# Kernel tuning notes

Measured on AMD Instinct MI355X. Metric: run time of the kernel, lower is better.

## Reference

```python
import jax, jax.numpy as jnp
import numpy as np

B, H, T, D = 4, 8, 4096, 64
NC = 64      # num_clusters
WSZ = 128    # window_size (== context_window_size)
MEM = 1      # num_mem_kv
EPS = 1e-5   # scatter_mean eps


def setup_inputs() -> dict:
    key = jax.random.key(0)
    kq, kk, kv, km, kmk, kmv = jax.random.split(key, 6)
    return {
        "q": jax.random.normal(kq, (B, H, T, D), jnp.float32),
        "k": jax.random.normal(kk, (B, H, T, D), jnp.float32),
        "v": jax.random.normal(kv, (B, H, T, D), jnp.float32),
        "means": jax.random.normal(km, (H, NC, D), jnp.float32),
        "mem_key": jax.random.normal(kmk, (H, NC, MEM, D), jnp.float32),
        "mem_value": jax.random.normal(kmv, (H, NC, MEM, D), jnp.float32),
    }


def reference(q, k, v, means, mem_key, mem_value):
    b, h, t, d = q.shape
    kv_t = k.shape[2]
    nc = means.shape[1]
    wsz = min(WSZ, t)
    kv_wsz = min(WSZ, kv_t)

    # --- kmeans routing (eval mode: no update, world_size=1) ---
    x = jnp.concatenate([q, k], axis=2)                       # (b,h,t+kv_t,d)
    norm = jnp.linalg.norm(x, axis=-1, keepdims=True)
    xn = x / jnp.maximum(norm, 1e-12)                          # F.normalize
    dists = jnp.einsum('bhld,hcd->bhlc', xn, means)            # (b,h,L,nc)
    buckets = jnp.argmax(dists, axis=-1)                       # (b,h,L)
    routed = means[jnp.arange(h)[None, :, None], buckets]      # (b,h,L,d)
    aux_loss = jnp.mean((xn - routed) ** 2)                    # mse / world_size(=1)

    dists = jax.lax.stop_gradient(dists)                       # torch no_grad
    q_dists, k_dists = dists[:, :, :t], dists[:, :, t:]

    def top_idx(dd, w):
        # dd: (b,h,L,nc) -> per-cluster top-w token indices, (b,h,nc*w)
        _, idx = jax.lax.top_k(jnp.swapaxes(dd, -1, -2), w)    # (b,h,nc,w)
        return idx.reshape(idx.shape[0], idx.shape[1], -1)

    indices = top_idx(q_dists, wsz)                            # (b,h,nc*wsz)
    kv_indices = top_idx(k_dists, kv_wsz)

    gather = lambda arr, idx: jnp.take_along_axis(arr, idx[..., None], axis=2)
    qg = gather(q, indices).reshape(b, h, nc, wsz, d)
    kg = gather(k, kv_indices).reshape(b, h, nc, kv_wsz, d)
    vg = gather(v, kv_indices).reshape(b, h, nc, kv_wsz, d)

    m_k = jnp.broadcast_to(mem_key[None], (b,) + mem_key.shape)
    m_v = jnp.broadcast_to(mem_value[None], (b,) + mem_value.shape)
    kg = jnp.concatenate([m_k, kg], axis=3)                    # (b,h,nc,MEM+kv_wsz,d)
    vg = jnp.concatenate([m_v, vg], axis=3)

    dots = jnp.einsum('bhnid,bhnjd->bhnij', qg, kg) * (d ** -0.5)
    attn = jax.nn.softmax(dots, axis=-1)
    bo = jnp.einsum('bhnij,bhnjd->bhnid', attn, vg)            # (b,h,nc,wsz,d)
    so = bo.reshape(b, h, nc * wsz, d)

    # scatter_mean back to token positions
    bi = jnp.arange(b)[:, None, None]
    hi = jnp.arange(h)[None, :, None]
    numer = jnp.zeros((b, h, t, d), q.dtype).at[bi, hi, indices].add(so)
    denom = jnp.zeros((b, h, t, d), q.dtype).at[bi, hi, indices].add(jnp.ones_like(so))
    out = numer / (denom + EPS)
    return out, aux_loss
```

## Files before the change

kernel.cpp:

```cpp
#include <hip/hip_runtime.h>
#include <math.h>

#define BB 4
#define HH 8
#define TT 4096
#define DD 64
#define NCC 64
#define WSZW 128
#define TPK 160
#define MEMN 1
#define KVW (MEMN + WSZW)
constexpr float EPSF = 1e-5f;
constexpr float SCALE = 0.125f;

typedef __attribute__((ext_vector_type(8))) short bf16x8;
typedef __attribute__((ext_vector_type(4))) float f32x4;

static __device__ __forceinline__ unsigned int pk2(float a, float b) {
    unsigned int r;
    asm("v_cvt_pk_bf16_f32 %0, %1, %2" : "=v"(r) : "v"(a), "v"(b));
    return r;
}
static __device__ __forceinline__ bf16x8 pack8(float4 a, float4 b) {
    union { unsigned int u[4]; bf16x8 v; } r;
    r.u[0] = pk2(a.x, a.y); r.u[1] = pk2(a.z, a.w);
    r.u[2] = pk2(b.x, b.y); r.u[3] = pk2(b.z, b.w);
    return r.v;
}
static __device__ __forceinline__ unsigned mono16(unsigned u) {
    return (u ^ ((u & 0x8000u) ? 0xFFFFu : 0x8000u)) & 0xFFFFu;
}
static __device__ __forceinline__ unsigned long long mono64(double d) {
    unsigned long long b = (unsigned long long)__double_as_longlong(d);
    return b ^ (((long long)b < 0) ? ~0ULL : 0x8000000000000000ULL);
}
static __device__ __forceinline__ float bf2f(unsigned short u) {
    return __uint_as_float(((unsigned)u) << 16);
}

__global__ __launch_bounds__(256, 4) void dists_kernel(
    const float* __restrict__ q, const float* __restrict__ k,
    const float* __restrict__ means,
    unsigned short* __restrict__ distsQ, unsigned short* __restrict__ distsK,
    float* __restrict__ aux_part, double* __restrict__ invn,
    int* __restrict__ counts)
{
    __shared__ __align__(16) unsigned short mhS[64 * 64];
    __shared__ __align__(16) unsigned short mlS[64 * 64];
    __shared__ __align__(16) unsigned short xhS[64 * 64];
    __shared__ __align__(16) unsigned short xlS[64 * 64];
    __shared__ float mqS[64];
    __shared__ float ssnS[64];
    __shared__ float wMaxS[64 * 5];
    __shared__ int   wIdxS[64 * 5];

    const int chunks = (2 * TT) / 64;
    int bid0 = blockIdx.x;
    int bid = (bid0 & 7) * 512 + (bid0 >> 3);
    int bh = bid / chunks;
    int chunk = bid % chunks;
    int h = bh % HH;
    bool isQ = chunk < (TT / 64);
    int tbase = (isQ ? chunk : chunk - 64) * 64;
    const float* src = (isQ ? q : k) + ((size_t)bh * TT + tbase) * DD;
    unsigned short* dst = isQ ? distsQ : distsK;
    double* invdst = invn + (isQ ? 0 : (size_t)BB * HH * TT) + (size_t)bh * TT + tbase;

    int tid = threadIdx.x;

    if (tid < 32) counts[(size_t)bid0 * 32 + tid] = 0;

    int row = tid >> 2, part = tid & 3;

    {
        const float* mp = means + ((size_t)h * NCC + row) * DD + part * 16;
        float f[16];
        float msq = 0.f;
        #pragma unroll
        for (int i = 0; i < 4; ++i) {
            float4 va = *(const float4*)(mp + i * 4);
            f[i*4] = va.x; f[i*4+1] = va.y; f[i*4+2] = va.z; f[i*4+3] = va.w;
            msq += va.x*va.x + va.y*va.y + va.z*va.z + va.w*va.w;
        }
        msq += __shfl_xor(msq, 1);
        msq += __shfl_xor(msq, 2);
        if (part == 0) mqS[row] = msq;
        #pragma unroll
        for (int cc = 0; cc < 2; ++cc) {
            unsigned hw[4], lw[4];
            #pragma unroll
            for (int j2 = 0; j2 < 4; ++j2) {
                float a = f[cc*8 + j2*2], b = f[cc*8 + j2*2 + 1];
                unsigned p = pk2(a, b);
                float ha = __uint_as_float(p << 16);
                float hb = __uint_as_float(p & 0xFFFF0000u);
                hw[j2] = p; lw[j2] = pk2(a - ha, b - hb);
            }
            int ch = part * 2 + cc;
            int phys = ch ^ (row & 7);
            *reinterpret_cast<uint4*>(&mhS[row * 64 + phys * 8]) = (uint4){hw[0],hw[1],hw[2],hw[3]};
            *reinterpret_cast<uint4*>(&mlS[row * 64 + phys * 8]) = (uint4){lw[0],lw[1],lw[2],lw[3]};
        }
    }
    {
        const float* xp = src + (size_t)row * DD + part * 16;
        float f[16];
        double ssd = 0.0;
        #pragma unroll
        for (int i = 0; i < 4; ++i) {
            float4 va = *(const float4*)(xp + i * 4);
            f[i*4] = va.x; f[i*4+1] = va.y; f[i*4+2] = va.z; f[i*4+3] = va.w;
            ssd += (double)va.x*va.x + (double)va.y*va.y
                 + (double)va.z*va.z + (double)va.w*va.w;
        }
        ssd += __shfl_xor(ssd, 1);
        ssd += __shfl_xor(ssd, 2);
        double invd = 1.0 / fmax(sqrt(ssd), 1e-12);
        if (part == 0) {
            invdst[row] = invd;
            ssnS[row] = (float)(ssd * invd * invd);
        }
        float inv = (float)invd;
        #pragma unroll
        for (int i = 0; i < 16; ++i) f[i] *= inv;
        #pragma unroll
        for (int cc = 0; cc < 2; ++cc) {
            unsigned hw[4], lw[4];
            #pragma unroll
            for (int j2 = 0; j2 < 4; ++j2) {
                float a = f[cc*8 + j2*2], b = f[cc*8 + j2*2 + 1];
                unsigned p = pk2(a, b);
                float ha = __uint_as_float(p << 16);
                float hb = __uint_as_float(p & 0xFFFF0000u);
                hw[j2] = p; lw[j2] = pk2(a - ha, b - hb);
            }
            int ch = part * 2 + cc;
            int phys = ch ^ (row & 7);
            *reinterpret_cast<uint4*>(&xhS[row * 64 + phys * 8]) = (uint4){hw[0],hw[1],hw[2],hw[3]};
            *reinterpret_cast<uint4*>(&xlS[row * 64 + phys * 8]) = (uint4){lw[0],lw[1],lw[2],lw[3]};
        }
    }
    __syncthreads();

    int l = tid & 63, w = tid >> 6;
    int lr = l & 15, lg = l >> 4;

    bf16x8 mhF[2], mlF[2];
    #pragma unroll
    for (int ks = 0; ks < 2; ++ks) {
        int r2 = w * 16 + lr;
        int phys = (ks * 4 + lg) ^ (r2 & 7);
        mhF[ks] = *reinterpret_cast<const bf16x8*>(&mhS[r2 * 64 + phys * 8]);
        mlF[ks] = *reinterpret_cast<const bf16x8*>(&mlS[r2 * 64 + phys * 8]);
    }

    f32x4 accT[4];
    size_t rowb = (size_t)(bh * NCC) * TT;
    #pragma unroll
    for (int tt = 0; tt < 4; ++tt) {
        bf16x8 xhF[2], xlF[2];
        #pragma unroll
        for (int ks = 0; ks < 2; ++ks) {
            int r2 = tt * 16 + lr;
            int phys = (ks * 4 + lg) ^ (r2 & 7);
            xhF[ks] = *reinterpret_cast<const bf16x8*>(&xhS[r2 * 64 + phys * 8]);
            xlF[ks] = *reinterpret_cast<const bf16x8*>(&xlS[r2 * 64 + phys * 8]);
        }
        f32x4 a = (f32x4){0.f, 0.f, 0.f, 0.f};
        #pragma unroll
        for (int ks = 0; ks < 2; ++ks)
            a = __builtin_amdgcn_mfma_f32_16x16x32_bf16(mhF[ks], xhF[ks], a, 0, 0, 0);
        #pragma unroll
        for (int ks = 0; ks < 2; ++ks)
            a = __builtin_amdgcn_mfma_f32_16x16x32_bf16(mhF[ks], xlF[ks], a, 0, 0, 0);
        #pragma unroll
        for (int ks = 0; ks < 2; ++ks)
            a = __builtin_amdgcn_mfma_f32_16x16x32_bf16(mlF[ks], xhF[ks], a, 0, 0, 0);
        accT[tt] = a;
        #pragma unroll
        for (int r2 = 0; r2 < 4; ++r2) {
            int c = w * 16 + lg * 4 + r2;
            dst[rowb + (size_t)c * TT + tbase + tt * 16 + lr] =
                (unsigned short)(pk2(a[r2], a[r2]) & 0xFFFFu);
        }
    }

    #pragma unroll
    for (int tt = 0; tt < 4; ++tt) {
        float bv = accT[tt][0]; int bc = w * 16 + lg * 4;
        #pragma unroll
        for (int r2 = 1; r2 < 4; ++r2)
            if (accT[tt][r2] > bv) { bv = accT[tt][r2]; bc = w * 16 + lg * 4 + r2; }
        #pragma unroll
        for (int off = 16; off <= 32; off <<= 1) {
            float ov = __shfl_xor(bv, off);
            int   oc = __shfl_xor(bc, off);
            if (ov > bv || (ov == bv && oc < bc)) { bv = ov; bc = oc; }
        }
        if (lg == 0) {
            wMaxS[(tt * 16 + lr) * 5 + w] = bv;
            wIdxS[(tt * 16 + lr) * 5 + w] = bc;
        }
    }
    __syncthreads();

    if (tid < 64) {
        float bv = -1e30f; int bc = 0;
        #pragma unroll
        for (int w2 = 0; w2 < 4; ++w2) {
            float ov = wMaxS[tid * 5 + w2];
            int   oc = wIdxS[tid * 5 + w2];
            if (ov > bv || (ov == bv && oc < bc)) { bv = ov; bc = oc; }
        }
        float auxv = ssnS[tid] + mqS[bc] - 2.f * bv;
        #pragma unroll
        for (int off = 32; off; off >>= 1) auxv += __shfl_xor(auxv, off);
        if (tid == 0) aux_part[bid] = auxv;
    }
}

__global__ __launch_bounds__(512) void topk_kernel(
    const unsigned short* __restrict__ dists, int* __restrict__ idxOut)
{
    int row = blockIdx.x;
    const unsigned short* dv = dists + (size_t)row * TT;
    int t = threadIdx.x;
    int lane = t & 63, w = t >> 6;

    unsigned u[8];
    {
        uint4 a = *(const uint4*)(dv + t * 8);
        unsigned ws[4] = {a.x, a.y, a.z, a.w};
        #pragma unroll
        for (int i = 0; i < 4; ++i) {
            u[i*2]   = mono16(ws[i] & 0xFFFFu);
            u[i*2+1] = mono16(ws[i] >> 16);
        }
    }

    __shared__ int hist[4096];
    __shared__ int wtot[8];
    __shared__ int binSel, tgtS;
    __shared__ int nGtS, posS, eqPos;

    int target = TPK;

    {
        int4* hz = (int4*)&hist[t * 8];
        hz[0] = (int4){0,0,0,0}; hz[1] = (int4){0,0,0,0};
        __syncthreads();
        #pragma unroll
        for (int j = 0; j < 8; ++j) atomicAdd(&hist[u[j] >> 4], 1);
        __syncthreads();
        int cnt[8], ls[8];
        {
            const int4* hp = (const int4*)&hist[t * 8];
            int4 c0 = hp[0], c1 = hp[1];
            cnt[0]=c0.x; cnt[1]=c0.y; cnt[2]=c0.z; cnt[3]=c0.w;
            cnt[4]=c1.x; cnt[5]=c1.y; cnt[6]=c1.z; cnt[7]=c1.w;
        }
        int run = 0;
        #pragma unroll
        for (int i = 7; i >= 0; --i) { run += cnt[i]; ls[i] = run; }
        int S = run;
        #pragma unroll
        for (int off = 1; off < 64; off <<= 1) {
            int o = __shfl_down(S, off);
            if (lane + off < 64) S += o;
        }
        if (lane == 0) wtot[w] = S;
        __syncthreads();
        int after = 0;
        for (int ww = w + 1; ww < 8; ++ww) after += wtot[ww];
        int St1 = S - run + after;
        #pragma unroll
        for (int i = 0; i < 8; ++i) {
            int sfxb = ls[i] + St1;
            if (sfxb >= target && sfxb - cnt[i] < target) {
                binSel = t * 8 + i; tgtS = target - (sfxb - cnt[i]);
            }
        }
        __syncthreads();
    }
    unsigned prefix12 = (unsigned)binSel;
    target = tgtS;
    __syncthreads();

    if (t < 16) hist[t] = 0;
    __syncthreads();
    #pragma unroll
    for (int j = 0; j < 8; ++j)
        if ((u[j] >> 4) == prefix12) atomicAdd(&hist[u[j] & 0xF], 1);
    __syncthreads();
    if (t < 16) {
        int cnt = hist[t];
        int S = cnt;
        #pragma unroll
        for (int off = 1; off < 16; off <<= 1) {
            int o = __shfl_down(S, off);
            if (t + off < 16) S += o;
        }
        if (S >= target && S - cnt < target) binSel = t;
    }
    __syncthreads();
    unsigned pivot = (prefix12 << 4) | (unsigned)binSel;

    if (t == 0) { nGtS = 0; posS = 0; eqPos = 0; }
    __syncthreads();
    int myg = 0;
    #pragma unroll
    for (int j = 0; j < 8; ++j) myg += (u[j] > pivot) ? 1 : 0;
    if (myg) atomicAdd(&nGtS, myg);
    __syncthreads();
    int n_gt = nGtS;
    int n_need = TPK - n_gt;
    int* out = idxOut + (size_t)row * TPK;
    #pragma unroll
    for (int j = 0; j < 8; ++j) {
        if (u[j] > pivot) {
            int p = atomicAdd(&posS, 1);
            out[p] = t * 8 + j;
        } else if (u[j] == pivot) {
            int p = atomicAdd(&eqPos, 1);
            if (p < n_need) out[n_gt + p] = t * 8 + j;
        }
    }
}

__global__ __launch_bounds__(640) void rescore_kernel(
    const float* __restrict__ q, const float* __restrict__ k,
    const float* __restrict__ means, const double* __restrict__ invn,
    const int* __restrict__ candQ, const int* __restrict__ candK,
    int* __restrict__ idxQ, int* __restrict__ idxK,
    int* __restrict__ counts)
{
    int bid = blockIdx.x;
    int rid = (bid & 7) * 512 + (bid >> 3);
    int side = rid >> 11;
    int row = rid & 2047;
    int c = row & (NCC - 1);
    int bh = row >> 6;
    int h = bh % HH;

    const int* cand = (side ? candK : candQ) + (size_t)row * TPK;
    int* outIdx     = (side ? idxK : idxQ) + (size_t)row * WSZW;
    const float* xbase = (side ? k : q) + (size_t)bh * TT * DD;
    const double* invp = invn + (side ? (size_t)BB * HH * TT : 0) + (size_t)bh * TT;

    __shared__ double   mD[DD];
    __shared__ unsigned hiS[TPK];
    __shared__ unsigned loS[TPK];
    __shared__ int      kiS[TPK];

    int tid = threadIdx.x;
    if (tid < DD) mD[tid] = (double)means[((size_t)h * NCC + c) * DD + tid];
    __syncthreads();

    int g = tid >> 2;
    int qt = tid & 3;
    int tok = cand[g];
    const float* xp = xbase + (size_t)tok * DD + qt * 16;
    double inv = invp[tok];
    double d0 = 0.0, d1 = 0.0;
    #pragma unroll
    for (int i = 0; i < 2; ++i) {
        float4 va = *(const float4*)(xp + i * 4);
        int d = qt * 16 + i * 4;
        d0 += (double)va.x * mD[d]   + (double)va.y * mD[d+1]
            + (double)va.z * mD[d+2] + (double)va.w * mD[d+3];
    }
    #pragma unroll
    for (int i = 2; i < 4; ++i) {
        float4 va = *(const float4*)(xp + i * 4);
        int d = qt * 16 + i * 4;
        d1 += (double)va.x * mD[d]   + (double)va.y * mD[d+1]
            + (double)va.z * mD[d+2] + (double)va.w * mD[d+3];
    }
    double dot = d0 + d1;
    dot += __shfl_xor(dot, 1); dot += __shfl_xor(dot, 2);
    double v = dot * inv;
    unsigned long long key = mono64(v);
    unsigned myhi = (unsigned)(key >> 32), mylo = (unsigned)key;
    if (qt == 0) { hiS[g] = myhi; loS[g] = mylo; kiS[g] = tok; }
    __syncthreads();

    int rk = 0, eq = 0;
    #pragma unroll 8
    for (int i = 0; i < TPK / 4; ++i) {
        unsigned hj = hiS[qt * (TPK / 4) + i];
        rk += (hj > myhi) ? 1 : 0;
        eq += (hj == myhi) ? 1 : 0;
    }
    rk += __shfl_xor(rk, 1); rk += __shfl_xor(rk, 2);
    eq += __shfl_xor(eq, 1); eq += __shfl_xor(eq, 2);

    if (eq > 1) {
        int rk2 = 0;
        for (int i = 0; i < TPK / 4; ++i) {
            int j = qt * (TPK / 4) + i;
            unsigned hj = hiS[j];
            if (hj > myhi) rk2++;
            else if (hj == myhi) {
                unsigned lj = loS[j];
                if (lj > mylo || (lj == mylo && kiS[j] < tok)) rk2++;
            }
        }
        rk2 += __shfl_xor(rk2, 1); rk2 += __shfl_xor(rk2, 2);
        rk = rk2;
    }

    if (qt == 0 && rk < WSZW) {
        outIdx[rk] = tok;
        if (side == 0) atomicAdd(&counts[bh * TT + tok], 1);
    }
}

__global__ __launch_bounds__(512, 8) void attn_scanfill_kernel(
    const float* __restrict__ q, const float* __restrict__ k, const float* __restrict__ v,
    const float* __restrict__ mem_key, const float* __restrict__ mem_value,
    const int* __restrict__ idxQ, const int* __restrict__ idxK,
    unsigned short* __restrict__ so,
    const int* __restrict__ counts, int* __restrict__ offs, int* __restrict__ csr,
    const float* __restrict__ auxp, float* __restrict__ out)
{
    __shared__ __align__(16) unsigned char smemRaw[38144];
    int bid = blockIdx.x;

    if (bid >= 2048) {
        int bh = bid - 2048;
        int t = threadIdx.x;
        int lane = t & 63, w = t >> 6;
        int* offsL = (int*)smemRaw;
        int* curL  = (int*)(smemRaw + 16384);
        int* wsum  = (int*)(smemRaw + 32768);
        float* auxW = (float*)(smemRaw + 32800);

        float s = 0.f;
        if (bh == 0)
            for (int i = t; i < 4096; i += 512) s += auxp[i];
        #pragma unroll
        for (int off = 32; off; off >>= 1) s += __shfl_xor(s, off);
        if (lane == 0) auxW[w] = s;
        __syncthreads();
        if (bh == 0 && t == 0) {
            float a = 0.f;
            #pragma unroll
            for (int i = 0; i < 8; ++i) a += auxW[i];
            out[(size_t)BB * HH * TT * DD] =
                a * (1.0f / (float)(BB * HH * 2 * TT * DD));
        }

        const int* cb = counts + (size_t)bh * TT;
        int* ob = offs + (size_t)bh * TT;
        int loc[8]; int sum = 0;
        #pragma unroll
        for (int i = 0; i < 8; ++i) { loc[i] = sum; sum += cb[t * 8 + i]; }
        int incl = sum;
        #pragma unroll
        for (int off = 1; off < 64; off <<= 1) {
            int o = __shfl_up(incl, off);
            if (lane >= off) incl += o;
        }
        if (lane == 63) wsum[w] = incl;
        __syncthreads();
        if (t < 8) {
            int v2 = wsum[t];
            int inc2 = v2;
            #pragma unroll
            for (int off = 1; off < 8; off <<= 1) {
                int o = __shfl_up(inc2, off);
                if (t >= off) inc2 += o;
            }
            wsum[t] = inc2 - v2;
        }
        __syncthreads();
        int ex = wsum[w] + incl - sum;
        #pragma unroll
        for (int i = 0; i < 8; ++i) {
            int o = ex + loc[i];
            ob[t * 8 + i] = o;
            offsL[t * 8 + i] = o;
            curL[t * 8 + i] = 0;
        }
        __syncthreads();

        const int* iq = idxQ + ((size_t)bh << 13);
        int* cs = csr + ((size_t)bh << 13);
        for (int i = t; i < 8192; i += 512) {
            int tok = iq[i];
            int p = offsL[tok] + atomicAdd(&curL[tok], 1);
            cs[p] = i;
        }
        return;
    }

    unsigned short* KsS = (unsigned short*)smemRaw;
    unsigned short* VtS = (unsigned short*)(smemRaw + 16640);

    int blk = (bid & 7) * 256 + (bid >> 3);
    int c = blk % NCC;
    int bh = blk / NCC;
    int h = bh % HH;

    int tid = threadIdx.x;
    int w = tid >> 6, l = tid & 63;
    int lr = l & 15, lg = l >> 4;

    const float* memK = mem_key   + ((size_t)h * NCC + c) * (MEMN * DD);
    const float* memV = mem_value + ((size_t)h * NCC + c) * (MEMN * DD);

    int stRow[3], stCh[3];
    const float *vsrcR[3], *ksrcR[3];
    #pragma unroll
    for (int s = 0; s < 3; ++s) {
        int idx = tid + s * 512;
        stRow[s] = idx >> 3; stCh[s] = idx & 7;
        vsrcR[s] = nullptr; ksrcR[s] = nullptr;
        if (idx < 1280 && stRow[s] < KVW) {
            if (stRow[s] == 0) { vsrcR[s] = memV; ksrcR[s] = memK; }
            else {
                int tk = idxK[(size_t)blk * WSZW + stRow[s] - 1];
                vsrcR[s] = v + ((size_t)bh * TT + tk) * DD;
                ksrcR[s] = k + ((size_t)bh * TT + tk) * DD;
            }
        }
    }

    bf16x8 qf[2];
    {
        int tq = idxQ[(size_t)blk * WSZW + w * 16 + lr];
        const float* qp = q + ((size_t)bh * TT + tq) * DD;
        #pragma unroll
        for (int ks = 0; ks < 2; ++ks) {
            float4 a = *(const float4*)(qp + ks * 32 + lg * 8);
            float4 b = *(const float4*)(qp + ks * 32 + lg * 8 + 4);
            qf[ks] = pack8(a, b);
        }
    }

    uint4 vw[3];
    #pragma unroll
    for (int s = 0; s < 3; ++s) {
        vw[s] = (uint4){0,0,0,0};
        if (vsrcR[s]) {
            float4 a = *(const float4*)(vsrcR[s] + stCh[s] * 8);
            float4 b = *(const float4*)(vsrcR[s] + stCh[s] * 8 + 4);
            vw[s].x = pk2(a.x, a.y); vw[s].y = pk2(a.z, a.w);
            vw[s].z = pk2(b.x, b.y); vw[s].w = pk2(b.z, b.w);
        }
    }
    uint4 kw[3];
    #pragma unroll
    for (int s = 0; s < 3; ++s) {
        kw[s] = (uint4){0,0,0,0};
        if (ksrcR[s]) {
            float4 a = *(const float4*)(ksrcR[s] + stCh[s] * 8);
            float4 b = *(const float4*)(ksrcR[s] + stCh[s] * 8 + 4);
            kw[s].x = pk2(a.x, a.y); kw[s].y = pk2(a.z, a.w);
            kw[s].z = pk2(b.x, b.y); kw[s].w = pk2(b.z, b.w);
        }
    }

    #pragma unroll
    for (int s = 0; s < 3; ++s)
        if (vsrcR[s])
            *reinterpret_cast<uint4*>(
                &KsS[stRow[s] * 64 + ((stCh[s] ^ (stRow[s] & 7)) * 8)]) = vw[s];
    __syncthreads();

    unsigned short vreg[3][8];
    #pragma unroll
    for (int s = 0; s < 3; ++s) {
        int idx = tid + s * 512;
        if (idx < 1280) {
            int d = idx & 63, rowblk = idx >> 6;
            #pragma unroll
            for (int i = 0; i < 8; ++i) {
                int row = rowblk * 8 + i;
                int pr = (row < KVW) ? row : 128;
                vreg[s][i] = KsS[pr * 64 + (((d >> 3) ^ (pr & 7)) * 8) + (d & 7)];
            }
        }
    }
    __syncthreads();

    #pragma unroll
    for (int s = 0; s < 3; ++s) {
        int idx = tid + s * 512;
        if (idx < 1280) {
            int d = idx & 63, rowblk = idx >> 6;
            uint4 ow;
            ow.x = (unsigned)vreg[s][0] | ((unsigned)vreg[s][1] << 16);
            ow.y = (unsigned)vreg[s][2] | ((unsigned)vreg[s][3] << 16);
            ow.z = (unsigned)vreg[s][4] | ((unsigned)vreg[s][5] << 16);
            ow.w = (unsigned)vreg[s][6] | ((unsigned)vreg[s][7] << 16);
            *reinterpret_cast<uint4*>(&VtS[d * 168 + rowblk * 8]) = ow;
        }
    }
    #pragma unroll
    for (int s = 0; s < 3; ++s)
        if (ksrcR[s])
            *reinterpret_cast<uint4*>(
                &KsS[stRow[s] * 64 + ((stCh[s] ^ (stRow[s] & 7)) * 8)]) = kw[s];
    __syncthreads();

    f32x4 acc[4];
    #pragma unroll
    for (int dt = 0; dt < 4; ++dt) acc[dt] = (f32x4){0.f, 0.f, 0.f, 0.f};
    float s_sum = 0.f;

    int src0 = lr + ((lg & 1) * 2) * 16;
    int src1 = src0 + 16;
    bool hi = (lg >> 1) != 0;

    for (int kb = 0; kb < 5; ++kb) {
        bf16x8 kf[2][2];
        #pragma unroll
        for (int kvt = 0; kvt < 2; ++kvt)
            #pragma unroll
            for (int ks = 0; ks < 2; ++ks) {
                int row = kb * 32 + kvt * 16 + lr;
                int pr = (row < KVW) ? row : 128;
                int phys = (ks * 4 + lg) ^ (pr & 7);
                kf[kvt][ks] = *reinterpret_cast<const bf16x8*>(&KsS[pr * 64 + phys * 8]);
            }
        __builtin_amdgcn_s_setprio(1);
        unsigned pk[2][2];
        #pragma unroll
        for (int kvt = 0; kvt < 2; ++kvt) {
            f32x4 sf = __builtin_amdgcn_mfma_f32_16x16x32_bf16(
                kf[kvt][0], qf[0], (f32x4){0.f,0.f,0.f,0.f}, 0, 0, 0);
            sf = __builtin_amdgcn_mfma_f32_16x16x32_bf16(kf[kvt][1], qf[1], sf, 0, 0, 0);
            float e[4];
            #pragma unroll
            for (int r = 0; r < 4; ++r) {
                int kv = kb * 32 + kvt * 16 + lg * 4 + r;
                e[r] = (kv < KVW) ? __expf(sf[r] * SCALE) : 0.f;
                s_sum += e[r];
            }
            pk[kvt][0] = pk2(e[0], e[1]);
            pk[kvt][1] = pk2(e[2], e[3]);
        }
        unsigned a00 = __shfl(pk[0][0], src0), a01 = __shfl(pk[0][1], src0);
        unsigned a10 = __shfl(pk[1][0], src0), a11 = __shfl(pk[1][1], src0);
        unsigned b00 = __shfl(pk[0][0], src1), b01 = __shfl(pk[0][1], src1);
        unsigned b10 = __shfl(pk[1][0], src1), b11 = __shfl(pk[1][1], src1);
        union { unsigned u[4]; bf16x8 v; } pu;
        pu.u[0] = hi ? a10 : a00;
        pu.u[1] = hi ? a11 : a01;
        pu.u[2] = hi ? b10 : b00;
        pu.u[3] = hi ? b11 : b01;
        #pragma unroll
        for (int dt = 0; dt < 4; ++dt) {
            bf16x8 vf = *reinterpret_cast<const bf16x8*>(
                &VtS[(dt * 16 + lr) * 168 + kb * 32 + lg * 8]);
            acc[dt] = __builtin_amdgcn_mfma_f32_16x16x32_bf16(pu.v, vf, acc[dt], 0, 0, 0);
        }
        __builtin_amdgcn_s_setprio(0);
    }

    s_sum += __shfl_xor(s_sum, 16);
    s_sum += __shfl_xor(s_sum, 32);
    float sinv[4];
    #pragma unroll
    for (int r = 0; r < 4; ++r)
        sinv[r] = 1.f / __shfl(s_sum, lg * 4 + r);

    #pragma unroll
    for (int r = 0; r < 4; ++r) {
        int row = w * 16 + lg * 4 + r;
        unsigned short* op = so + (((size_t)blk * WSZW + row) * DD);
        #pragma unroll
        for (int dt = 0; dt < 4; ++dt) {
            float ov = acc[dt][r] * sinv[r];
            op[dt * 16 + lr] = (unsigned short)(pk2(ov, ov) & 0xFFFFu);
        }
    }
}

__global__ __launch_bounds__(256) void reduce_kernel(
    const unsigned short* __restrict__ so, const int* __restrict__ counts,
    const int* __restrict__ offs, const int* __restrict__ csr,
    float* __restrict__ out)
{
    int b0 = blockIdx.x;
    int b = (b0 & 7) * 4096 + (b0 >> 3);
    int gt = b * 4 + (threadIdx.x >> 6);
    int lane = threadIdx.x & 63;
    int bh = gt >> 12;
    int n = counts[gt];
    int st = offs[gt];
    const int* cs = csr + ((size_t)bh << 13);
    const unsigned short* sob = so + (((size_t)bh << 13) * DD);
    float acc = 0.f;
    int j = 0;
    for (; j + 2 <= n; j += 2) {
        int s0 = cs[st + j], s1 = cs[st + j + 1];
        float v0 = bf2f(sob[(size_t)s0 * DD + lane]);
        float v1 = bf2f(sob[(size_t)s1 * DD + lane]);
        acc += v0 + v1;
    }
    if (j < n) acc += bf2f(sob[(size_t)cs[st + j] * DD + lane]);
    out[(size_t)gt * DD + lane] = acc / ((float)n + EPSF);
}

extern "C" void kernel_launch(void* const* d_in, const int* in_sizes, int n_in,
                              void* d_out, int out_size, void* d_ws, size_t ws_size,
                              hipStream_t stream) {
    const float* q        = (const float*)d_in[0];
    const float* k        = (const float*)d_in[1];
    const float* v        = (const float*)d_in[2];
    const float* means    = (const float*)d_in[3];
    const float* mem_key  = (const float*)d_in[4];
    const float* mem_val  = (const float*)d_in[5];
    float* out = (float*)d_out;

    const size_t nRows = (size_t)BB * HH * NCC;
    const size_t nTok  = (size_t)BB * HH * TT;
    const size_t nDist = (size_t)BB * HH * NCC * TT;
    unsigned short* distsQ = (unsigned short*)d_ws;
    unsigned short* distsK = distsQ + nDist;
    unsigned short* so     = distsQ;
    int*   idxQ   = (int*)(distsK + nDist);
    int*   idxK   = idxQ + nRows * WSZW;
    int*   counts = idxK + nRows * WSZW;
    float* auxp   = (float*)(counts + nTok);
    int*   offs   = (int*)(auxp + 4096);
    int*   csr    = offs + nTok;
    int*   candQ  = csr + nTok * 2;
    int*   candK  = candQ + nRows * TPK;
    uintptr_t ip  = (uintptr_t)(candK + nRows * TPK);
    ip = (ip + 15) & ~(uintptr_t)15;
    double* invn  = (double*)ip;

    dists_kernel<<<dim3(BB * HH * (2 * TT / 64)), dim3(256), 0, stream>>>(
        q, k, means, distsQ, distsK, auxp, invn, counts);
    topk_kernel<<<dim3((unsigned)(2 * nRows)), dim3(512), 0, stream>>>(distsQ, candQ);
    rescore_kernel<<<dim3((unsigned)(2 * nRows)), dim3(640), 0, stream>>>(
        q, k, means, invn, candQ, candK, idxQ, idxK, counts);
    attn_scanfill_kernel<<<dim3((unsigned)(nRows + BB * HH)), dim3(512), 0, stream>>>(
        q, k, v, mem_key, mem_val, idxQ, idxK, so,
        counts, offs, csr, auxp, out);
    reduce_kernel<<<dim3((unsigned)(nTok / 4)), dim3(256), 0, stream>>>(
        so, counts, offs, csr, out);
}
```

Measured before the change: 160.1 us.

## Fuse radix top-k candidate selection with double-precision rescoring kernel

```diff
diff --git a/kernel.cpp b/kernel.cpp
--- a/kernel.cpp
+++ b/kernel.cpp
@@ -219,118 +219,10 @@
     }
 }
 
-__global__ __launch_bounds__(512) void topk_kernel(
-    const unsigned short* __restrict__ dists, int* __restrict__ idxOut)
-{
-    int row = blockIdx.x;
-    const unsigned short* dv = dists + (size_t)row * TT;
-    int t = threadIdx.x;
-    int lane = t & 63, w = t >> 6;
-
-    unsigned u[8];
-    {
-        uint4 a = *(const uint4*)(dv + t * 8);
-        unsigned ws[4] = {a.x, a.y, a.z, a.w};
-        #pragma unroll
-        for (int i = 0; i < 4; ++i) {
-            u[i*2]   = mono16(ws[i] & 0xFFFFu);
-            u[i*2+1] = mono16(ws[i] >> 16);
-        }
-    }
-
-    __shared__ int hist[4096];
-    __shared__ int wtot[8];
-    __shared__ int binSel, tgtS;
-    __shared__ int nGtS, posS, eqPos;
-
-    int target = TPK;
-
-    {
-        int4* hz = (int4*)&hist[t * 8];
-        hz[0] = (int4){0,0,0,0}; hz[1] = (int4){0,0,0,0};
-        __syncthreads();
-        #pragma unroll
-        for (int j = 0; j < 8; ++j) atomicAdd(&hist[u[j] >> 4], 1);
-        __syncthreads();
-        int cnt[8], ls[8];
-        {
-            const int4* hp = (const int4*)&hist[t * 8];
-            int4 c0 = hp[0], c1 = hp[1];
-            cnt[0]=c0.x; cnt[1]=c0.y; cnt[2]=c0.z; cnt[3]=c0.w;
-            cnt[4]=c1.x; cnt[5]=c1.y; cnt[6]=c1.z; cnt[7]=c1.w;
-        }
-        int run = 0;
-        #pragma unroll
-        for (int i = 7; i >= 0; --i) { run += cnt[i]; ls[i] = run; }
-        int S = run;
-        #pragma unroll
-        for (int off = 1; off < 64; off <<= 1) {
-            int o = __shfl_down(S, off);
-            if (lane + off < 64) S += o;
-        }
-        if (lane == 0) wtot[w] = S;
-        __syncthreads();
-        int after = 0;
-        for (int ww = w + 1; ww < 8; ++ww) after += wtot[ww];
-        int St1 = S - run + after;
-        #pragma unroll
-        for (int i = 0; i < 8; ++i) {
-            int sfxb = ls[i] + St1;
-            if (sfxb >= target && sfxb - cnt[i] < target) {
-                binSel = t * 8 + i; tgtS = target - (sfxb - cnt[i]);
-            }
-        }
-        __syncthreads();
-    }
-    unsigned prefix12 = (unsigned)binSel;
-    target = tgtS;
-    __syncthreads();
-
-    if (t < 16) hist[t] = 0;
-    __syncthreads();
-    #pragma unroll
-    for (int j = 0; j < 8; ++j)
-        if ((u[j] >> 4) == prefix12) atomicAdd(&hist[u[j] & 0xF], 1);
-    __syncthreads();
-    if (t < 16) {
-        int cnt = hist[t];
-        int S = cnt;
-        #pragma unroll
-        for (int off = 1; off < 16; off <<= 1) {
-            int o = __shfl_down(S, off);
-            if (t + off < 16) S += o;
-        }
-        if (S >= target && S - cnt < target) binSel = t;
-    }
-    __syncthreads();
-    unsigned pivot = (prefix12 << 4) | (unsigned)binSel;
-
-    if (t == 0) { nGtS = 0; posS = 0; eqPos = 0; }
-    __syncthreads();
-    int myg = 0;
-    #pragma unroll
-    for (int j = 0; j < 8; ++j) myg += (u[j] > pivot) ? 1 : 0;
-    if (myg) atomicAdd(&nGtS, myg);
-    __syncthreads();
-    int n_gt = nGtS;
-    int n_need = TPK - n_gt;
-    int* out = idxOut + (size_t)row * TPK;
-    #pragma unroll
-    for (int j = 0; j < 8; ++j) {
-        if (u[j] > pivot) {
-            int p = atomicAdd(&posS, 1);
-            out[p] = t * 8 + j;
-        } else if (u[j] == pivot) {
-            int p = atomicAdd(&eqPos, 1);
-            if (p < n_need) out[n_gt + p] = t * 8 + j;
-        }
-    }
-}
-
-__global__ __launch_bounds__(640) void rescore_kernel(
+__global__ __launch_bounds__(512) void topk_rescore_kernel(
+    const unsigned short* __restrict__ dists,
     const float* __restrict__ q, const float* __restrict__ k,
     const float* __restrict__ means, const double* __restrict__ invn,
-    const int* __restrict__ candQ, const int* __restrict__ candK,
     int* __restrict__ idxQ, int* __restrict__ idxK,
     int* __restrict__ counts)
 {
@@ -342,76 +234,190 @@
     int bh = row >> 6;
     int h = bh % HH;
 
-    const int* cand = (side ? candK : candQ) + (size_t)row * TPK;
-    int* outIdx     = (side ? idxK : idxQ) + (size_t)row * WSZW;
+    const unsigned short* dv = dists + ((size_t)side * 2048 + row) * TT;
+    int* outIdx = (side ? idxK : idxQ) + (size_t)row * WSZW;
     const float* xbase = (side ? k : q) + (size_t)bh * TT * DD;
     const double* invp = invn + (side ? (size_t)BB * HH * TT : 0) + (size_t)bh * TT;
 
+    __shared__ int hist[4096];
+    __shared__ int wtot[8];
+    __shared__ int binSel, tgtS;
+    __shared__ int nGtS, posS, eqPos;
+    __shared__ int candL[TPK];
     __shared__ double   mD[DD];
     __shared__ unsigned hiS[TPK];
     __shared__ unsigned loS[TPK];
     __shared__ int      kiS[TPK];
 
-    int tid = threadIdx.x;
-    if (tid < DD) mD[tid] = (double)means[((size_t)h * NCC + c) * DD + tid];
-    __syncthreads();
-
-    int g = tid >> 2;
-    int qt = tid & 3;
-    int tok = cand[g];
-    const float* xp = xbase + (size_t)tok * DD + qt * 16;
-    double inv = invp[tok];
-    double d0 = 0.0, d1 = 0.0;
-    #pragma unroll
-    for (int i = 0; i < 2; ++i) {
-        float4 va = *(const float4*)(xp + i * 4);
-        int d = qt * 16 + i * 4;
-        d0 += (double)va.x * mD[d]   + (double)va.y * mD[d+1]
-            + (double)va.z * mD[d+2] + (double)va.w * mD[d+3];
-    }
-    #pragma unroll
-    for (int i = 2; i < 4; ++i) {
-        float4 va = *(const float4*)(xp + i * 4);
-        int d = qt * 16 + i * 4;
-        d1 += (double)va.x * mD[d]   + (double)va.y * mD[d+1]
-            + (double)va.z * mD[d+2] + (double)va.w * mD[d+3];
-    }
-    double dot = d0 + d1;
-    dot += __shfl_xor(dot, 1); dot += __shfl_xor(dot, 2);
-    double v = dot * inv;
-    unsigned long long key = mono64(v);
-    unsigned myhi = (unsigned)(key >> 32), mylo = (unsigned)key;
-    if (qt == 0) { hiS[g] = myhi; loS[g] = mylo; kiS[g] = tok; }
-    __syncthreads();
-
-    int rk = 0, eq = 0;
-    #pragma unroll 8
-    for (int i = 0; i < TPK / 4; ++i) {
-        unsigned hj = hiS[qt * (TPK / 4) + i];
-        rk += (hj > myhi) ? 1 : 0;
-        eq += (hj == myhi) ? 1 : 0;
-    }
-    rk += __shfl_xor(rk, 1); rk += __shfl_xor(rk, 2);
-    eq += __shfl_xor(eq, 1); eq += __shfl_xor(eq, 2);
-
-    if (eq > 1) {
-        int rk2 = 0;
-        for (int i = 0; i < TPK / 4; ++i) {
-            int j = qt * (TPK / 4) + i;
-            unsigned hj = hiS[j];
-            if (hj > myhi) rk2++;
-            else if (hj == myhi) {
-                unsigned lj = loS[j];
-                if (lj > mylo || (lj == mylo && kiS[j] < tok)) rk2++;
-            }
-        }
-        rk2 += __shfl_xor(rk2, 1); rk2 += __shfl_xor(rk2, 2);
-        rk = rk2;
-    }
-
-    if (qt == 0 && rk < WSZW) {
-        outIdx[rk] = tok;
-        if (side == 0) atomicAdd(&counts[bh * TT + tok], 1);
+    int t = threadIdx.x;
+    int lane = t & 63, w = t >> 6;
+
+    if (t < DD) mD[t] = (double)means[((size_t)h * NCC + c) * DD + t];
+
+    unsigned u[8];
+    {
+        uint4 a = *(const uint4*)(dv + t * 8);
+        unsigned ws[4] = {a.x, a.y, a.z, a.w};
+        #pragma unroll
+        for (int i = 0; i < 4; ++i) {
+            u[i*2]   = mono16(ws[i] & 0xFFFFu);
+            u[i*2+1] = mono16(ws[i] >> 16);
+        }
+    }
+
+    int target = TPK;
+
+    {
+        int4* hz = (int4*)&hist[t * 8];
+        hz[0] = (int4){0,0,0,0}; hz[1] = (int4){0,0,0,0};
+        __syncthreads();
+        #pragma unroll
+        for (int j = 0; j < 8; ++j) atomicAdd(&hist[u[j] >> 4], 1);
+        __syncthreads();
+        int cnt[8], ls[8];
+        {
+            const int4* hp = (const int4*)&hist[t * 8];
+            int4 c0 = hp[0], c1 = hp[1];
+            cnt[0]=c0.x; cnt[1]=c0.y; cnt[2]=c0.z; cnt[3]=c0.w;
+            cnt[4]=c1.x; cnt[5]=c1.y; cnt[6]=c1.z; cnt[7]=c1.w;
+        }
+        int run = 0;
+        #pragma unroll
+        for (int i = 7; i >= 0; --i) { run += cnt[i]; ls[i] = run; }
+        int S = run;
+        #pragma unroll
+        for (int off = 1; off < 64; off <<= 1) {
+            int o = __shfl_down(S, off);
+            if (lane + off < 64) S += o;
+        }
+        if (lane == 0) wtot[w] = S;
+        __syncthreads();
+        int after = 0;
+        for (int ww = w + 1; ww < 8; ++ww) after += wtot[ww];
+        int St1 = S - run + after;
+        #pragma unroll
+        for (int i = 0; i < 8; ++i) {
+            int sfxb = ls[i] + St1;
+            if (sfxb >= target && sfxb - cnt[i] < target) {
+                binSel = t * 8 + i; tgtS = target - (sfxb - cnt[i]);
+            }
+        }
+        __syncthreads();
+    }
+    unsigned prefix12 = (unsigned)binSel;
+    target = tgtS;
+    __syncthreads();
+
+    if (t < 16) hist[t] = 0;
+    __syncthreads();
+    #pragma unroll
+    for (int j = 0; j < 8; ++j)
+        if ((u[j] >> 4) == prefix12) atomicAdd(&hist[u[j] & 0xF], 1);
+    __syncthreads();
+    if (t < 16) {
+        int cnt = hist[t];
+        int S = cnt;
+        #pragma unroll
+        for (int off = 1; off < 16; off <<= 1) {
+            int o = __shfl_down(S, off);
+            if (t + off < 16) S += o;
+        }
+        if (S >= target && S - cnt < target) binSel = t;
+    }
+    __syncthreads();
+    unsigned pivot = (prefix12 << 4) | (unsigned)binSel;
+
+    if (t == 0) { nGtS = 0; posS = 0; eqPos = 0; }
+    __syncthreads();
+    int myg = 0;
+    #pragma unroll
+    for (int j = 0; j < 8; ++j) myg += (u[j] > pivot) ? 1 : 0;
+    if (myg) atomicAdd(&nGtS, myg);
+    __syncthreads();
+    int n_gt = nGtS;
+    int n_need = TPK - n_gt;
+    #pragma unroll
+    for (int j = 0; j < 8; ++j) {
+        if (u[j] > pivot) {
+            int p = atomicAdd(&posS, 1);
+            candL[p] = t * 8 + j;
+        } else if (u[j] == pivot) {
+            int p = atomicAdd(&eqPos, 1);
+            if (p < n_need) candL[n_gt + p] = t * 8 + j;
+        }
+    }
+    __syncthreads();
+
+    int qt = t & 3;
+    #pragma unroll
+    for (int base = 0; base < TPK; base += 128) {
+        int g = base + (t >> 2);
+        if (g < TPK) {
+            int tok = candL[g];
+            const float* xp = xbase + (size_t)tok * DD + qt * 16;
+            double inv = invp[tok];
+            double d0 = 0.0, d1 = 0.0;
+            #pragma unroll
+            for (int i = 0; i < 2; ++i) {
+                float4 va = *(const float4*)(xp + i * 4);
+                int d = qt * 16 + i * 4;
+                d0 += (double)va.x * mD[d]   + (double)va.y * mD[d+1]
+                    + (double)va.z * mD[d+2] + (double)va.w * mD[d+3];
+            }
+            #pragma unroll
+            for (int i = 2; i < 4; ++i) {
+                float4 va = *(const float4*)(xp + i * 4);
+                int d = qt * 16 + i * 4;
+                d1 += (double)va.x * mD[d]   + (double)va.y * mD[d+1]
+                    + (double)va.z * mD[d+2] + (double)va.w * mD[d+3];
+            }
+            double dot = d0 + d1;
+            dot += __shfl_xor(dot, 1); dot += __shfl_xor(dot, 2);
+            double vv = dot * inv;
+            unsigned long long key = mono64(vv);
+            if (qt == 0) {
+                hiS[g] = (unsigned)(key >> 32);
+                loS[g] = (unsigned)key;
+                kiS[g] = tok;
+            }
+        }
+    }
+    __syncthreads();
+
+    #pragma unroll
+    for (int base = 0; base < TPK; base += 128) {
+        int g = base + (t >> 2);
+        if (g < TPK) {
+            unsigned myhi = hiS[g], mylo = loS[g];
+            int tok = kiS[g];
+            int rk = 0, eq = 0;
+            #pragma unroll 8
+            for (int i = 0; i < TPK / 4; ++i) {
+                unsigned hj = hiS[qt * (TPK / 4) + i];
+                rk += (hj > myhi) ? 1 : 0;
+                eq += (hj == myhi) ? 1 : 0;
+            }
+            rk += __shfl_xor(rk, 1); rk += __shfl_xor(rk, 2);
+            eq += __shfl_xor(eq, 1); eq += __shfl_xor(eq, 2);
+            if (eq > 1) {
+                int rk2 = 0;
+                for (int i = 0; i < TPK / 4; ++i) {
+                    int j = qt * (TPK / 4) + i;
+                    unsigned hj = hiS[j];
+                    if (hj > myhi) rk2++;
+                    else if (hj == myhi) {
+                        unsigned lj = loS[j];
+                        if (lj > mylo || (lj == mylo && kiS[j] < tok)) rk2++;
+                    }
+                }
+                rk2 += __shfl_xor(rk2, 1); rk2 += __shfl_xor(rk2, 2);
+                rk = rk2;
+            }
+            if (qt == 0 && rk < WSZW) {
+                outIdx[rk] = tok;
+                if (side == 0) atomicAdd(&counts[bh * TT + tok], 1);
+            }
+        }
     }
 }
 
@@ -727,17 +733,14 @@
     float* auxp   = (float*)(counts + nTok);
     int*   offs   = (int*)(auxp + 4096);
     int*   csr    = offs + nTok;
-    int*   candQ  = csr + nTok * 2;
-    int*   candK  = candQ + nRows * TPK;
-    uintptr_t ip  = (uintptr_t)(candK + nRows * TPK);
+    uintptr_t ip  = (uintptr_t)(csr + nTok * 2);
     ip = (ip + 15) & ~(uintptr_t)15;
     double* invn  = (double*)ip;
 
     dists_kernel<<<dim3(BB * HH * (2 * TT / 64)), dim3(256), 0, stream>>>(
         q, k, means, distsQ, distsK, auxp, invn, counts);
-    topk_kernel<<<dim3((unsigned)(2 * nRows)), dim3(512), 0, stream>>>(distsQ, candQ);
-    rescore_kernel<<<dim3((unsigned)(2 * nRows)), dim3(640), 0, stream>>>(
-        q, k, means, invn, candQ, candK, idxQ, idxK, counts);
+    topk_rescore_kernel<<<dim3((unsigned)(2 * nRows)), dim3(512), 0, stream>>>(
+        distsQ, q, k, means, invn, idxQ, idxK, counts);
     attn_scanfill_kernel<<<dim3((unsigned)(nRows + BB * HH)), dim3(512), 0, stream>>>(
         q, k, v, mem_key, mem_val, idxQ, idxK, so,
         counts, offs, csr, auxp, out);
```

New measurement: 159.0 us, median of 2. About the same (-0.7%).
